# Kernel optimization log

Hardware: AMD Instinct MI355X
Metric: run time of the kernel (lower is better)

The kernel has to match this reference:

```python
import jax, jax.numpy as jnp
import numpy as np
from jax.scipy.linalg import cholesky, solve_triangular, cho_solve

N, M, D = 16384, 2048, 8
VAR, LS = 1.0, 0.5      # RBF kernel hyperparameters (same for kernel_f and kernel_g)
JITTER = 1e-6
BATCH_RATE = 1.0
HALF_LOG_2PI = 0.5 * float(np.log(2.0 * np.pi))


def rbf(x1, x2):
    # K[i,j] = VAR * exp(-||x1_i - x2_j||^2 / (2 LS^2))
    d2 = (jnp.sum(x1 * x1, 1)[:, None] + jnp.sum(x2 * x2, 1)[None, :]
          - 2.0 * (x1 @ x2.T))
    return VAR * jnp.exp(-0.5 * d2 / (LS * LS))


def setup_inputs() -> dict:
    key = jax.random.key(0)
    ks = jax.random.split(key, 7)
    x = jax.random.normal(ks[0], (N, D), dtype=jnp.float32)
    y = jax.random.normal(ks[1], (N, 1), dtype=jnp.float32)
    z = 2.0 * jax.random.uniform(ks[2], (M, D), dtype=jnp.float32) - 1.0  # inducing inputs in [-1,1]^D
    q_m_f = 0.5 * jax.random.normal(ks[3], (M, 1), dtype=jnp.float32)
    q_m_g = 0.5 * jax.random.normal(ks[4], (M, 1), dtype=jnp.float32)
    # Cholesky-like params: identity plus small strictly-lower noise -> PD covariance
    q_L_f = jnp.eye(M, dtype=jnp.float32) + 0.01 * jnp.tril(
        jax.random.normal(ks[5], (M, M), dtype=jnp.float32), -1)
    q_L_g = jnp.eye(M, dtype=jnp.float32) + 0.01 * jnp.tril(
        jax.random.normal(ks[6], (M, M), dtype=jnp.float32), -1)
    return {"x": x, "y": y, "z": z, "q_m_f": q_m_f, "q_L_f": q_L_f,
            "q_m_g": q_m_g, "q_L_g": q_L_g}


def _gp_marginals_and_kl(x, z, q_m, q_L_raw):
    """Marginal posterior mean/var at x and KL(q(u)||p(u)) for one sparse GP."""
    L_S = jnp.tril(q_L_raw)                     # [M,M]
    Kuu = rbf(z, z) + JITTER * jnp.eye(M, dtype=x.dtype)
    Lk = cholesky(Kuu, lower=True)
    Kfu = rbf(x, z)                             # [N,M]
    # A = Kfu @ Kuu^{-1}
    A = cho_solve((Lk, True), Kfu.T).T          # [N,M]
    m = (A @ q_m)[:, 0]                         # [N]
    # diag(Kff + A (S - Kuu) A^T) = diag(Kff) + diag(A S A^T) - diag(Kfu A^T)
    S = L_S @ L_S.T
    diag_Kff = jnp.full((x.shape[0],), VAR, dtype=x.dtype)
    v = diag_Kff + jnp.sum((A @ S) * A, axis=1) - jnp.sum(A * Kfu, axis=1)
    # KL(N(q_m, S) || N(0, Kuu))
    alpha = solve_triangular(Lk, q_m, lower=True)       # Kuu^{-1/2} m
    W = solve_triangular(Lk, L_S, lower=True)           # Kuu^{-1/2} L_S
    logdet_K = 2.0 * jnp.sum(jnp.log(jnp.diag(Lk)))
    logdet_S = 2.0 * jnp.sum(jnp.log(jnp.abs(jnp.diag(L_S))))
    kl = 0.5 * (jnp.sum(W * W) + jnp.sum(alpha * alpha)
                - jnp.asarray(M, x.dtype) + logdet_K - logdet_S)
    return m, v, kl


def reference(x, y, z, q_m_f, q_L_f, q_m_g, q_L_g):
    m_f, v_f, kl_f = _gp_marginals_and_kl(x, z, q_m_f, q_L_f)
    m_g, v_g, kl_g = _gp_marginals_and_kl(x, z, q_m_g, q_L_g)
    yv = y[:, 0]
    # HetGaussian variational expectation (Saul et al. 2016):
    # E_q[log N(y | f, exp(g))] per point
    expectation = (-HALF_LOG_2PI - 0.5 * m_g
                   - 0.5 * ((yv - m_f) ** 2 + v_f) * jnp.exp(-m_g + 0.5 * v_g))
    elbo = BATCH_RATE * jnp.sum(expectation) - (kl_f + kl_g)
    return -elbo
```

## Files before the change

kernel.cpp:

```cpp
#include <hip/hip_runtime.h>
#include <math.h>

#define NN 16384
#define MM 2048
#define DD 8
#define NB 32
#define GRIDN 256
#define SZB ((size_t)16777216)

constexpr float HLOG2PI = 0.91893853320467274178f;

using short8  = __attribute__((ext_vector_type(8))) short;
using float4v = __attribute__((ext_vector_type(4))) float;

__device__ __forceinline__ float4v f4zero(){ float4v v; v[0]=0.f; v[1]=0.f; v[2]=0.f; v[3]=0.f; return v; }

__device__ __forceinline__ void bfsplit(float v, short& h, short& lo){
  unsigned b = __float_as_uint(v);
  h = (short)(b >> 16);
  float hf = __uint_as_float(b & 0xFFFF0000u);
  lo = (short)(__float_as_uint(v - hf) >> 16);
}
__device__ __forceinline__ float bf2f(short s){
  return __uint_as_float(((unsigned)(unsigned short)s) << 16);
}
__device__ __forceinline__ float4v mfma3(short8 ah, short8 al, short8 bh, short8 bl, float4v c){
  c = __builtin_amdgcn_mfma_f32_16x16x32_bf16(ah, bh, c, 0, 0, 0);
  c = __builtin_amdgcn_mfma_f32_16x16x32_bf16(ah, bl, c, 0, 0, 0);
  c = __builtin_amdgcn_mfma_f32_16x16x32_bf16(al, bh, c, 0, 0, 0);
  return c;
}

__device__ __forceinline__ void gbar(int* cnt, int* flag, int& gen){
  __syncthreads();
  if (threadIdx.x == 0){
    ++gen;
    __builtin_amdgcn_fence(__ATOMIC_RELEASE, "agent");
    int old = __hip_atomic_fetch_add(cnt, 1, __ATOMIC_RELAXED, __HIP_MEMORY_SCOPE_AGENT);
    if (old == gen*GRIDN - 1){
      __builtin_amdgcn_fence(__ATOMIC_ACQ_REL, "agent");
      __hip_atomic_store(flag, gen, __ATOMIC_RELAXED, __HIP_MEMORY_SCOPE_AGENT);
    } else {
      while (__hip_atomic_load(flag, __ATOMIC_RELAXED, __HIP_MEMORY_SCOPE_AGENT) < gen)
        __builtin_amdgcn_s_sleep(8);
    }
    __builtin_amdgcn_fence(__ATOMIC_ACQUIRE, "agent");
  }
  __syncthreads();
}

__device__ __forceinline__ float block_reduce(float v, float* scratch){
  int lane = threadIdx.x & 63;
  int w    = threadIdx.x >> 6;
  #pragma unroll
  for (int off=32; off; off>>=1) v += __shfl_down(v, off, 64);
  __syncthreads();
  if (lane==0) scratch[w] = v;
  __syncthreads();
  float r = 0.f;
  if (threadIdx.x < 4) r = scratch[threadIdx.x];
  if (w==0){ r += __shfl_down(r, 2, 64); r += __shfl_down(r, 1, 64); }
  return r;
}

__device__ __forceinline__ void stage64(float (*S)[68], const float* __restrict__ g, int ld, int t){
  #pragma unroll
  for (int p=t; p<1024; p+=256)
    *(float4*)&S[p>>4][(p&15)*4] = *(const float4*)&g[(size_t)(p>>4)*ld + (p&15)*4];
}
__device__ __forceinline__ void tile_gemm_step(float acc[4][4], const float (*As)[68], const float (*Bs)[68], int tx, int ty){
  for (int k=0;k<64;++k){
    float ar[4], bc4[4];
    #pragma unroll
    for (int u=0;u<4;++u){ ar[u]=As[ty*4+u][k]; bc4[u]=Bs[k][tx*4+u]; }
    #pragma unroll
    for (int u=0;u<4;++u)
      #pragma unroll
      for (int v=0;v<4;++v) acc[u][v] += ar[u]*bc4[v];
  }
}
__device__ __forceinline__ void tile_syrk_step(float acc[4][4], const float (*P)[68], const float (*Q)[68], int tx, int ty){
  for (int k=0;k<64;++k){
    float pr[4], qc[4];
    #pragma unroll
    for (int u=0;u<4;++u){ pr[u]=P[ty*4+u][k]; qc[u]=Q[tx*4+u][k]; }
    #pragma unroll
    for (int u=0;u<4;++u)
      #pragma unroll
      for (int v=0;v<4;++v) acc[u][v] += pr[u]*qc[v];
  }
}

__device__ void factor64(float (*A)[68], float* __restrict__ lkd, float* __restrict__ sdg_, int d, int t){
  for (int j=0;j<64;++j){
    float ajj = A[j][j];
    float piv = sqrtf(fmaxf(ajj, 1e-20f));
    float rp  = 1.f/piv;
    float val = 0.f;
    if (t>j && t<64){ val = A[t][j]*rp; A[t][j]=val; }
    __syncthreads();
    if (t<64){
      if (t>j) for (int c=j+1;c<=t;++c) A[t][c] -= val*A[c][j];
      if (t==j){ A[j][j]=piv; sdg_[d*64+j]=rp; }
    }
    __syncthreads();
  }
  for (int p=t; p<4096; p+=256){ int i=p>>6, c=p&63;
    lkd[d*4096+p] = (c<=i)? A[i][c] : 0.f; }
}

__global__ __launch_bounds__(256) void factor_coop(
    const float* __restrict__ z,
    const float* __restrict__ qlf, const float* __restrict__ qlg,
    const float* __restrict__ qmf, const float* __restrict__ qmg,
    float* __restrict__ kuu, float* __restrict__ linv,
    float* __restrict__ wf, float* __restrict__ wg,
    float* __restrict__ af, float* __restrict__ ag,
    float* __restrict__ ptmp, float* __restrict__ lkdiag,
    float* __restrict__ sdg, int* __restrict__ cnt, int* __restrict__ flag)
{
  __shared__ float As[64][68];
  __shared__ float Bs[64][68];
  __shared__ float sd[64];
  const int bid = blockIdx.x, t = threadIdx.x;
  const int tx = t & 15, ty = t >> 4;
  int gen = 0;

  if (bid == 0){
    for (int p=t; p<128; p+=256){ int i=p>>1, h=p&1;
      *(float4*)&As[i][h*4] = *(const float4*)&z[(size_t)i*DD + h*4]; }
    __syncthreads();
    float kv[4][4];
    #pragma unroll
    for (int u=0;u<4;++u)
      #pragma unroll
      for (int v=0;v<4;++v){
        float d2=0.f;
        #pragma unroll
        for (int d=0;d<8;++d){ float df=As[ty*4+u][d]-As[tx*4+v][d]; d2+=df*df; }
        kv[u][v] = __expf(-2.f*d2) + ((ty*4+u)==(tx*4+v) ? 1e-6f : 0.f);
      }
    __syncthreads();
    #pragma unroll
    for (int u=0;u<4;++u)
      #pragma unroll
      for (int v=0;v<4;++v) As[ty*4+u][tx*4+v] = kv[u][v];
    __syncthreads();
    factor64(As, lkdiag, sdg, 0, t);
  } else {
    for (int idx=bid; idx<528; idx+=GRIDN-1){
      int r=0; while ((r+1)*(r+2)/2 <= idx) ++r;
      int c = idx - r*(r+1)/2;
      __syncthreads();
      for (int p=t; p<128; p+=256){ int i=p>>1, h=p&1;
        *(float4*)&As[i][h*4] = *(const float4*)&z[(size_t)(r*64+i)*DD + h*4];
        *(float4*)&Bs[i][h*4] = *(const float4*)&z[(size_t)(c*64+i)*DD + h*4]; }
      __syncthreads();
      #pragma unroll
      for (int u=0;u<4;++u){
        float4 o;
        float* ov = (float*)&o;
        #pragma unroll
        for (int v=0;v<4;++v){
          float d2=0.f;
          #pragma unroll
          for (int d=0;d<8;++d){ float df=As[ty*4+u][d]-Bs[tx*4+v][d]; d2+=df*df; }
          float val = __expf(-2.f*d2);
          if (r*64+ty*4+u == c*64+tx*4+v) val += 1e-6f;
          ov[v] = val;
        }
        *(float4*)&kuu[(size_t)(r*64+ty*4+u)*MM + c*64 + tx*4] = o;
      }
    }
  }
  gbar(cnt, flag, gen);

  for (int kb=0; kb<31; ++kb){
    int R = MM - (kb+1)*64;
    int nact = (R + 255) >> 8;
    if (bid < nact){
      for (int p=t; p<1024; p+=256)
        *(float4*)&As[p>>4][(p&15)*4] = *(const float4*)&lkdiag[kb*4096 + p*4];
      if (t < 64) sd[t] = sdg[kb*64 + t];
      __syncthreads();
      int row = (kb+1)*64 + bid*256 + t;
      if (row < MM){
        float xr[64];
        float* ap = kuu + (size_t)row*MM + kb*64;
        #pragma unroll
        for (int c4=0; c4<16; ++c4) *(float4*)&xr[c4*4] = *(const float4*)&ap[c4*4];
        #pragma unroll
        for (int j=0; j<64; ++j){
          float xj = xr[j]*sd[j];
          xr[j] = xj;
          #pragma unroll
          for (int c=j+1; c<64; ++c) xr[c] -= xj*As[c][j];
        }
        #pragma unroll
        for (int c4=0; c4<16; ++c4) *(float4*)&ap[c4*4] = *(float4*)&xr[c4*4];
      }
    }
    gbar(cnt, flag, gen);

    int T = NB-1 - kb;
    int ntiles = T*(T+1)/2;
    if (bid == 0){
      int bi = kb+1;
      stage64(As, kuu + (size_t)(bi*64)*MM + kb*64, MM, t);
      __syncthreads();
      float acc[4][4] = {};
      tile_syrk_step(acc, As, As, tx, ty);
      __syncthreads();
      #pragma unroll
      for (int u=0;u<4;++u)
        #pragma unroll
        for (int v=0;v<4;++v) Bs[ty*4+u][tx*4+v] = acc[u][v];
      __syncthreads();
      for (int p=t;p<1024;p+=256){
        int i=p>>4, c4=p&15;
        float4 kv = *(const float4*)&kuu[(size_t)(bi*64+i)*MM + bi*64 + c4*4];
        float4 bv = *(float4*)&Bs[i][c4*4];
        float4 o; o.x=kv.x-bv.x; o.y=kv.y-bv.y; o.z=kv.z-bv.z; o.w=kv.w-bv.w;
        *(float4*)&As[i][c4*4] = o;
      }
      __syncthreads();
      factor64(As, lkdiag, sdg, kb+1, t);
    } else {
      for (int idx=bid; idx<ntiles; idx+=GRIDN-1){
        int r=0; while ((r+1)*(r+2)/2 <= idx) ++r;
        int c = idx - r*(r+1)/2;
        int bi = kb+1+r, bc = kb+1+c;
        __syncthreads();
        stage64(As, kuu + (size_t)(bi*64)*MM + kb*64, MM, t);
        stage64(Bs, kuu + (size_t)(bc*64)*MM + kb*64, MM, t);
        __syncthreads();
        float acc[4][4] = {};
        tile_syrk_step(acc, As, Bs, tx, ty);
        #pragma unroll
        for (int u=0;u<4;++u){
          float4* dst = (float4*)&kuu[(size_t)(bi*64+ty*4+u)*MM + bc*64 + tx*4];
          float4 o = *dst;
          o.x-=acc[u][0]; o.y-=acc[u][1]; o.z-=acc[u][2]; o.w-=acc[u][3];
          *dst = o;
        }
      }
    }
    gbar(cnt, flag, gen);
  }

  if (bid < NB){
    stage64(As, lkdiag + bid*4096, 64, t);
    __syncthreads();
    if (t < 64){
      for (int j=0;j<64;++j){
        float s = (j==t)?1.f:0.f;
        for (int k=t;k<j;++k) s -= As[j][k]*Bs[k][t];
        Bs[j][t] = (j>=t)? s/As[j][j] : 0.f;
      }
    }
    __syncthreads();
    for (int p=t;p<1024;p+=256){ int i=p>>4, c4=p&15;
      *(float4*)&linv[(size_t)(bid*64+i)*MM + bid*64 + c4*4] = *(float4*)&Bs[i][c4*4]; }
  }
  gbar(cnt, flag, gen);

  for (int s=0; s<5; ++s){
    int nb = 1<<s, mc = 16>>s, b = 64<<s;
    int tiles = mc*nb*nb;
    for (int idx=bid; idx<tiles; idx+=GRIDN){
      int m = idx/(nb*nb), r2 = idx%(nb*nb);
      int ti = r2/nb, tj = r2%nb;
      int rb = m*2*nb + nb + ti, cb0 = m*2*nb;
      float acc[4][4]={};
      for (int k=tj; k<nb; ++k){
        __syncthreads();
        stage64(As, kuu  + (size_t)(rb*64)*MM + (cb0+k)*64, MM, t);
        stage64(Bs, linv + (size_t)((cb0+k)*64)*MM + (cb0+tj)*64, MM, t);
        __syncthreads();
        tile_gemm_step(acc, As, Bs, tx, ty);
      }
      float* pm = ptmp + (size_t)m*b*b;
      #pragma unroll
      for (int u=0;u<4;++u)
        *(float4*)&pm[(size_t)(ti*64+ty*4+u)*b + tj*64 + tx*4] =
            make_float4(acc[u][0],acc[u][1],acc[u][2],acc[u][3]);
    }
    gbar(cnt, flag, gen);
    for (int idx=bid; idx<tiles; idx+=GRIDN){
      int m = idx/(nb*nb), r2 = idx%(nb*nb);
      int ti = r2/nb, tj = r2%nb;
      int rb = m*2*nb + nb + ti;
      const float* pm = ptmp + (size_t)m*b*b;
      float acc[4][4]={};
      for (int k=0; k<=ti; ++k){
        __syncthreads();
        stage64(As, linv + (size_t)(rb*64)*MM + (m*2*nb+nb+k)*64, MM, t);
        stage64(Bs, pm + (size_t)(k*64)*b + tj*64, b, t);
        __syncthreads();
        tile_gemm_step(acc, As, Bs, tx, ty);
      }
      #pragma unroll
      for (int u=0;u<4;++u)
        *(float4*)&linv[(size_t)(rb*64+ty*4+u)*MM + (m*2*nb+tj)*64 + tx*4] =
            make_float4(-acc[u][0],-acc[u][1],-acc[u][2],-acc[u][3]);
    }
    gbar(cnt, flag, gen);
  }

  for (int idx=bid; idx<2*528; idx+=GRIDN){
    int gp = idx/528, rem = idx%528;
    int bi=0; while ((bi+1)*(bi+2)/2 <= rem) ++bi;
    int bj = rem - bi*(bi+1)/2;
    const float* ql = gp ? qlg : qlf;
    float* w        = gp ? wg  : wf;
    float acc[4][4]={};
    for (int bk=bj; bk<=bi; ++bk){
      __syncthreads();
      stage64(As, linv + (size_t)(bi*64)*MM + bk*64, MM, t);
      stage64(Bs, ql   + (size_t)(bk*64)*MM + bj*64, MM, t);
      __syncthreads();
      if (bk==bj){
        for (int p=t;p<4096;p+=256){ int i=p>>6, c=p&63; if (i<c) Bs[i][c]=0.f; }
        __syncthreads();
      }
      tile_gemm_step(acc, As, Bs, tx, ty);
    }
    #pragma unroll
    for (int u=0;u<4;++u)
      *(float4*)&w[(size_t)(bi*64+ty*4+u)*MM + bj*64 + tx*4] =
          make_float4(acc[u][0],acc[u][1],acc[u][2],acc[u][3]);
  }
  {
    int gw = bid*4 + (t>>6), l = t&63;
    for (int job=gw; job<4096; job+=GRIDN*4){
      int gp = job>>11, r = job&2047;
      const float* qm = gp ? qmg : qmf;
      float s=0.f;
      for (int c=l; c<=r; c+=64) s += linv[(size_t)r*MM+c]*qm[c];
      #pragma unroll
      for (int off=32; off; off>>=1) s += __shfl_down(s, off, 64);
      if (l==0) (gp ? ag : af)[r] = s;
    }
  }
}


__global__ __launch_bounds__(256) void zfrag_kernel(const float* __restrict__ z,
    short* __restrict__ zfh, short* __restrict__ zfl, float* __restrict__ zn2){
  int zr = blockIdx.x*256 + threadIdx.x;
  float v[DD]; float s = 0.f;
  #pragma unroll
  for (int d=0; d<DD; ++d){ v[d] = z[zr*DD + d]; s += v[d]*v[d]; }
  zn2[zr] = s;
  size_t base = (size_t)(zr >> 4)*512 + (zr & 15)*32;
  #pragma unroll
  for (int k=0; k<32; ++k){
    short h = 0, lo = 0;
    if (k < DD) bfsplit(v[k], h, lo);
    zfh[base + k] = h; zfl[base + k] = lo;
  }
}

__global__ __launch_bounds__(256) void red_small(const float* __restrict__ lkd,
    const float* __restrict__ qlf, const float* __restrict__ qlg,
    const float* __restrict__ af, const float* __restrict__ ag,
    float* __restrict__ scal){
  __shared__ float scratch[4];
  float ldk=0, ldf=0, ldg=0, a2f=0, a2g=0;
  for (int i=threadIdx.x;i<MM;i+=256){
    int kb = i>>6, r = i&63;
    ldk += __logf(lkd[kb*4096 + r*64 + r]);
    ldf += __logf(fabsf(qlf[(size_t)i*MM+i]));
    ldg += __logf(fabsf(qlg[(size_t)i*MM+i]));
    float v = af[i]; a2f += v*v;
    v = ag[i];       a2g += v*v;
  }
  float r;
  r = block_reduce(ldk, scratch); if (threadIdx.x==0) scal[0] = 2.f*r;
  r = block_reduce(ldf, scratch); if (threadIdx.x==0) scal[1] = 2.f*r;
  r = block_reduce(ldg, scratch); if (threadIdx.x==0) scal[2] = 2.f*r;
  r = block_reduce(a2f, scratch); if (threadIdx.x==0) scal[3] = r;
  r = block_reduce(a2g, scratch); if (threadIdx.x==0) scal[4] = r;
}

__global__ __launch_bounds__(256) void redw_kernel(const float* __restrict__ wf,
    const float* __restrict__ wg, float* __restrict__ scal){
  __shared__ float scratch[4];
  size_t start  = (size_t)blockIdx.x*256 + threadIdx.x;
  size_t stride = (size_t)gridDim.x*256;
  float sf=0, sg=0;
  for (size_t p=start;p<(size_t)MM*MM;p+=stride){
    float v=wf[p]; sf += v*v;
    v=wg[p];       sg += v*v;
  }
  float r = block_reduce(sf, scratch);
  if (threadIdx.x==0) atomicAdd(&scal[5], r);
  r = block_reduce(sg, scratch);
  if (threadIdx.x==0) atomicAdd(&scal[6], r);
}

__global__ void kl_kernel(const float* __restrict__ scal, float* __restrict__ out){
  float klf = 0.5f*(scal[5] + scal[3] - (float)MM + scal[0] - scal[1]);
  float klg = 0.5f*(scal[6] + scal[4] - (float)MM + scal[0] - scal[2]);
  out[0] += klf + klg;
}

__global__ __launch_bounds__(256) void split_rowmajor(const float* __restrict__ src,
    short* __restrict__ dh, short* __restrict__ dl){
  int p = blockIdx.x*256 + threadIdx.x;
  int chunk = p >> 9, wi = p & 511;
  int mo = chunk >> 6, ko = chunk & 63;
  int row = mo*16 + (wi >> 5), col = ko*32 + (wi & 31);
  float v = src[(size_t)row*MM + col];
  short h, lo; bfsplit(v, h, lo);
  dh[p] = h; dl[p] = lo;
}

__global__ __launch_bounds__(256) void split_transpose(const float* __restrict__ src,
    short* __restrict__ dh, short* __restrict__ dl){
  __shared__ float tile[32][33];
  int t = threadIdx.x;
  int mb = blockIdx.x, kb = blockIdx.y;
  #pragma unroll
  for (int k=0;k<4;++k){
    int idx = t + k*256;
    int lr = idx >> 5, lc = idx & 31;
    tile[lr][lc] = src[(size_t)(kb*32+lr)*MM + mb*32 + lc];
  }
  __syncthreads();
  #pragma unroll
  for (int e=0;e<4;++e){
    int p = t*4 + e;
    int c = p >> 9, wi = p & 511;
    int i = (wi >> 5) & 15, kk = wi & 31;
    float v = tile[kk][c*16 + i];
    short h, lo; bfsplit(v, h, lo);
    size_t gp = ((size_t)(mb*2 + c)*64 + kb)*512 + wi;
    dh[gp] = h; dl[gp] = lo;
  }
}

__global__ __launch_bounds__(256, 2) void tt_mfma(
    const float* __restrict__ x, const float* __restrict__ zn2,
    const short* __restrict__ zfh, const short* __restrict__ zfl,
    const short* __restrict__ lvh, const short* __restrict__ lvl,
    short* __restrict__ tth, short* __restrict__ ttl){
  __shared__ __align__(16) short lAh[8192], lAl[8192], lBh[8192], lBl[8192];
  int t = threadIdx.x;
  int l = t & 63, w = t >> 6;
  int istrip = blockIdx.x, bj2 = blockIdx.y;
  int li = l & 15, q = l >> 4;
  int lofs = li*32 + q*8;
  int wn4 = (w>>1)*4, wm4 = (w&1)*4;

  short8 xh[2], xl[2];
  float xn2v[8];
  {
    float xn2t[2];
    #pragma unroll
    for (int tn=0; tn<2; ++tn){
      int n = istrip*128 + w*32 + tn*16 + li;
      const float4* xp = (const float4*)(x + (size_t)n*DD);
      float4 p0 = xp[0], p1 = xp[1];
      float v[8] = {p0.x,p0.y,p0.z,p0.w,p1.x,p1.y,p1.z,p1.w};
      float s = 0.f;
      #pragma unroll
      for (int d=0; d<8; ++d) s += v[d]*v[d];
      xn2t[tn] = s;
      short8 hh, ll;
      #pragma unroll
      for (int j=0; j<8; ++j){
        short h=0, lo=0;
        if (q==0) bfsplit(v[j], h, lo);
        hh[j]=h; ll[j]=lo;
      }
      xh[tn]=hh; xl[tn]=ll;
    }
    #pragma unroll
    for (int tn=0; tn<2; ++tn)
      #pragma unroll
      for (int r=0; r<4; ++r)
        xn2v[tn*4+r] = __shfl(xn2t[tn], q*4 + r, 64);
  }

  float4v acc[4][4];
  #pragma unroll
  for (int i=0;i<4;++i)
    #pragma unroll
    for (int j=0;j<4;++j) acc[i][j] = f4zero();

  int nkt = 2*bj2 + 2;
  for (int bk=0; bk<nkt; ++bk){
    __syncthreads();
    {
      short8 zh[4], zl[4];
      float zt2[4];
      #pragma unroll
      for (int tz=0; tz<4; ++tz){
        size_t zo = (size_t)(bk*4 + tz)*512 + lofs;
        zh[tz] = *(const short8*)(zfh + zo);
        zl[tz] = *(const short8*)(zfl + zo);
        zt2[tz] = zn2[bk*64 + tz*16 + li];
      }
      #pragma unroll
      for (int tn=0; tn<2; ++tn){
        #pragma unroll
        for (int tz=0; tz<4; ++tz){
          float4v s4 = mfma3(xh[tn], xl[tn], zh[tz], zl[tz], f4zero());
          #pragma unroll
          for (int r=0; r<4; ++r){
            float e = __expf(4.f*s4[r] - 2.f*(xn2v[tn*4+r] + zt2[tz]));
            short h, lo; bfsplit(e, h, lo);
            int pos = ((w*2+tn)*2 + (tz>>1))*512 + (q*4+r)*32 + (tz&1)*16 + li;
            lAh[pos] = h; lAl[pos] = lo;
          }
        }
      }
    }
    #pragma unroll
    for (int c4 = t; c4 < 1024; c4 += 256){
      int ch = c4 >> 6, wdi = c4 & 63;
      size_t g = ((size_t)(bj2*8 + (ch>>1))*64 + (size_t)(bk*2 + (ch&1)))*64 + wdi;
      ((uint4*)lBh)[c4] = ((const uint4*)lvh)[g];
      ((uint4*)lBl)[c4] = ((const uint4*)lvl)[g];
    }
    __syncthreads();
    #pragma unroll
    for (int s=0; s<2; ++s){
      short8 ah[4], al[4], bh[4], bl[4];
      #pragma unroll
      for (int tn=0; tn<4; ++tn){
        int off = ((wn4+tn)*2 + s)*512 + lofs;
        ah[tn] = *(const short8*)&lAh[off];
        al[tn] = *(const short8*)&lAl[off];
      }
      #pragma unroll
      for (int tm=0; tm<4; ++tm){
        int off = ((wm4+tm)*2 + s)*512 + lofs;
        bh[tm] = *(const short8*)&lBh[off];
        bl[tm] = *(const short8*)&lBl[off];
      }
      #pragma unroll
      for (int tn=0; tn<4; ++tn)
        #pragma unroll
        for (int tm=0; tm<4; ++tm)
          acc[tn][tm] = mfma3(ah[tn], al[tn], bh[tm], bl[tm], acc[tn][tm]);
    }
  }
  #pragma unroll
  for (int tn=0; tn<4; ++tn){
    int no_g = istrip*8 + wn4 + tn;
    #pragma unroll
    for (int tm=0; tm<4; ++tm){
      int mo_g = bj2*4 + (w&1)*2 + (tm>>1);
      size_t cb = ((size_t)no_g*64 + mo_g)*512;
      #pragma unroll
      for (int r=0; r<4; ++r){
        short h, lo; bfsplit(acc[tn][tm][r], h, lo);
        size_t pos = cb + (q*4+r)*32 + (tm&1)*16 + li;
        tth[pos] = h; ttl[pos] = lo;
      }
    }
  }
}

__global__ __launch_bounds__(256) void lin_v2(const short* __restrict__ tth,
    const short* __restrict__ ttl, const float* __restrict__ af, const float* __restrict__ ag,
    float* __restrict__ t2, float* __restrict__ lf, float* __restrict__ lg){
  int t = threadIdx.x;
  int w = t >> 6, l = t & 63;
  int n = blockIdx.x*4 + w;
  int g = l >> 2, j = l & 3;
  float s2=0.f, sf=0.f, sg=0.f;
  #pragma unroll
  for (int it=0; it<4; ++it){
    int ck = g + it*16;
    size_t off = ((size_t)(n>>4)*64 + ck)*512 + (n&15)*32 + j*8;
    short8 h8 = *(const short8*)(tth + off);
    short8 l8 = *(const short8*)(ttl + off);
    int m0 = ck*32 + j*8;
    float4 a0 = *(const float4*)(af + m0), a1 = *(const float4*)(af + m0 + 4);
    float4 g0 = *(const float4*)(ag + m0), g1 = *(const float4*)(ag + m0 + 4);
    float av[8] = {a0.x,a0.y,a0.z,a0.w,a1.x,a1.y,a1.z,a1.w};
    float gv[8] = {g0.x,g0.y,g0.z,g0.w,g1.x,g1.y,g1.z,g1.w};
    #pragma unroll
    for (int e=0; e<8; ++e){
      float tv = bf2f(h8[e]) + bf2f(l8[e]);
      s2 += tv*tv; sf += tv*av[e]; sg += tv*gv[e];
    }
  }
  #pragma unroll
  for (int off=32; off; off>>=1){
    s2 += __shfl_down(s2, off, 64);
    sf += __shfl_down(sf, off, 64);
    sg += __shfl_down(sg, off, 64);
  }
  if (l==0){ t2[n] = s2; lf[n] = sf; lg[n] = sg; }
}

__global__ __launch_bounds__(256, 2) void quad_mfma(
    const short* __restrict__ tth, const short* __restrict__ ttl,
    const short* __restrict__ wfh, const short* __restrict__ wfl,
    const short* __restrict__ wgh, const short* __restrict__ wgl,
    float* __restrict__ vfq, float* __restrict__ vgq){
  __shared__ __align__(16) short lAh[8192], lAl[8192], lBh[8192], lBl[8192];
  int t = threadIdx.x, l = t & 63, w = t >> 6;
  int istrip = blockIdx.x, bj2 = blockIdx.y;
  const short* gbh = blockIdx.z ? wgh : wfh;
  const short* gbl = blockIdx.z ? wgl : wfl;
  float* vq = blockIdx.z ? vgq : vfq;
  int li = l & 15, q = l >> 4;
  int lofs = li*32 + q*8;
  int wn4 = (w>>1)*4, wm4 = (w&1)*4;

  float4v acc[4][4];
  #pragma unroll
  for (int i=0;i<4;++i)
    #pragma unroll
    for (int j=0;j<4;++j) acc[i][j] = f4zero();

  for (int bk=2*bj2; bk<32; ++bk){
    __syncthreads();
    #pragma unroll
    for (int c4 = t; c4 < 1024; c4 += 256){
      int ch = c4 >> 6, wdi = c4 & 63;
      size_t ga = ((size_t)(istrip*8 + (ch>>1))*64 + (size_t)(bk*2 + (ch&1)))*64 + wdi;
      ((uint4*)lAh)[c4] = ((const uint4*)tth)[ga];
      ((uint4*)lAl)[c4] = ((const uint4*)ttl)[ga];
      size_t gb = ((size_t)(bj2*8 + (ch>>1))*64 + (size_t)(bk*2 + (ch&1)))*64 + wdi;
      ((uint4*)lBh)[c4] = ((const uint4*)gbh)[gb];
      ((uint4*)lBl)[c4] = ((const uint4*)gbl)[gb];
    }
    __syncthreads();
    #pragma unroll
    for (int s=0; s<2; ++s){
      short8 ah[4], al[4], bh[4], bl[4];
      #pragma unroll
      for (int tn=0; tn<4; ++tn){
        int off = ((wn4+tn)*2 + s)*512 + lofs;
        ah[tn] = *(const short8*)&lAh[off];
        al[tn] = *(const short8*)&lAl[off];
      }
      #pragma unroll
      for (int tm=0; tm<4; ++tm){
        int off = ((wm4+tm)*2 + s)*512 + lofs;
        bh[tm] = *(const short8*)&lBh[off];
        bl[tm] = *(const short8*)&lBl[off];
      }
      #pragma unroll
      for (int tn=0; tn<4; ++tn)
        #pragma unroll
        for (int tm=0; tm<4; ++tm)
          acc[tn][tm] = mfma3(ah[tn], al[tn], bh[tm], bl[tm], acc[tn][tm]);
    }
  }
  float rs[16];
  #pragma unroll
  for (int tn=0; tn<4; ++tn)
    #pragma unroll
    for (int r=0; r<4; ++r){
      float s = 0.f;
      #pragma unroll
      for (int tm=0; tm<4; ++tm){ float v = acc[tn][tm][r]; s += v*v; }
      rs[tn*4+r] = s;
    }
  #pragma unroll
  for (int off=8; off; off>>=1)
    #pragma unroll
    for (int k=0; k<16; ++k) rs[k] += __shfl_down(rs[k], off, 16);
  if (li == 0){
    #pragma unroll
    for (int tn=0; tn<4; ++tn)
      #pragma unroll
      for (int r=0; r<4; ++r){
        int n = istrip*128 + (w>>1)*64 + tn*16 + q*4 + r;
        atomicAdd(&vq[n], rs[tn*4+r]);
      }
  }
}

__global__ __launch_bounds__(256) void final_kernel(const float* __restrict__ y,
    const float* __restrict__ t2, const float* __restrict__ lf, const float* __restrict__ lg,
    const float* __restrict__ vfq, const float* __restrict__ vgq, float* __restrict__ out){
  __shared__ float scratch[4];
  int i = blockIdx.x*256 + threadIdx.x;
  float mf = lf[i], mg = lg[i];
  float vf = 1.f + vfq[i] - t2[i];
  float vg = 1.f + vgq[i] - t2[i];
  float dy = y[i] - mf;
  float e = -HLOG2PI - 0.5f*mg - 0.5f*(dy*dy + vf)*__expf(-mg + 0.5f*vg);
  float r = block_reduce(e, scratch);
  if (threadIdx.x==0) atomicAdd(out, -r);
}

extern "C" void kernel_launch(void* const* d_in, const int* in_sizes, int n_in,
                              void* d_out, int out_size, void* d_ws, size_t ws_size,
                              hipStream_t stream){
  (void)in_sizes; (void)n_in; (void)out_size; (void)ws_size;
  const float* x   = (const float*)d_in[0];
  const float* y   = (const float*)d_in[1];
  const float* z   = (const float*)d_in[2];
  const float* qmf = (const float*)d_in[3];
  const float* qlf = (const float*)d_in[4];
  const float* qmg = (const float*)d_in[5];
  const float* qlg = (const float*)d_in[6];
  float* out = (float*)d_out;
  char* Bw = (char*)d_ws;

  float* kuu  = (float*)Bw;
  float* linv = (float*)(Bw + SZB);
  float* wf   = (float*)(Bw + 2*SZB);
  float* wg   = (float*)(Bw + 3*SZB);
  short* lvh  = (short*)Bw;
  short* lvl  = (short*)(Bw + SZB/2);
  short* wfh  = (short*)(Bw + SZB);
  short* wfl  = (short*)(Bw + SZB + SZB/2);
  short* wgh  = (short*)(Bw + 2*SZB);
  short* wgl  = (short*)(Bw + 2*SZB + SZB/2);
  short* tth  = (short*)(Bw + 3*SZB);
  short* ttl  = (short*)(Bw + 3*SZB + (size_t)NN*MM*2);
  float* ptmp   = (float*)(Bw + 4*SZB);
  float* lkdiag = (float*)(Bw + 4*SZB + (size_t)4194304);
  float* sdg    = (float*)(Bw + 4*SZB + (size_t)4194304 + (size_t)524288);
  float* sm   = (float*)(Bw + 3*SZB + (size_t)NN*MM*4);
  float* af = sm;          float* ag = af + MM;
  float* t2 = ag + MM;     float* lf = t2 + NN;   float* lg = lf + NN;
  float* vfq = lg + NN;    float* vgq = vfq + NN; float* scal = vgq + NN;
  int*   cnt  = (int*)(scal + 8);
  int*   flag = (int*)(scal + 40);
  float* zn2 = scal + 48;
  short* zfh = (short*)(zn2 + MM);
  short* zfl = zfh + MM*32;

  hipMemsetAsync(out, 0, sizeof(float), stream);
  hipMemsetAsync(vfq, 0, (size_t)(2*NN + 48)*sizeof(float), stream);
  hipMemsetAsync(wf,  0, 2*SZB, stream);
  hipMemsetAsync(linv,0, SZB,   stream);

  zfrag_kernel<<<MM/256, 256, 0, stream>>>(z, zfh, zfl, zn2);

  factor_coop<<<GRIDN, 256, 0, stream>>>(z, qlf, qlg, qmf, qmg,
                                         kuu, linv, wf, wg, af, ag,
                                         ptmp, lkdiag, sdg, cnt, flag);

  red_small<<<1, 256, 0, stream>>>(lkdiag, qlf, qlg, af, ag, scal);
  redw_kernel<<<512, 256, 0, stream>>>(wf, wg, scal);
  kl_kernel<<<1, 1, 0, stream>>>(scal, out);

  split_rowmajor<<<MM*MM/256, 256, 0, stream>>>(linv, lvh, lvl);
  split_transpose<<<dim3(MM/32, MM/32), 256, 0, stream>>>(wf, wfh, wfl);
  split_transpose<<<dim3(MM/32, MM/32), 256, 0, stream>>>(wg, wgh, wgl);

  tt_mfma<<<dim3(NN/128, MM/128), 256, 0, stream>>>(x, zn2, zfh, zfl, lvh, lvl, tth, ttl);
  lin_v2<<<NN/4, 256, 0, stream>>>(tth, ttl, af, ag, t2, lf, lg);
  quad_mfma<<<dim3(NN/128, MM/128, 2), 256, 0, stream>>>(tth, ttl, wfh, wfl, wgh, wgl, vfq, vgq);
  final_kernel<<<NN/256, 256, 0, stream>>>(y, t2, lf, lg, vfq, vgq, out);
}
```

Measured before the change: 4.743 ms.

## Use hierarchical per-XCD grid barrier, register Cholesky diag, dedicated first inverse level

Replaces the flat global atomic grid barrier with a two-level barrier that first counts blocks per XCD (read from the hardware XCC_ID register) and then across XCDs. This cuts contention on a single counter across the many barriers of the cooperative Cholesky kernel. It also rewrites the 64x64 diagonal block factorization to run in registers with wave shuffles instead of shared memory with per-column syncthreads, and computes the first level of the triangular-inverse recursion with a specialized two-GEMM tile path, which removes one barrier. The cost is a startup barrier used to discover block placement, plus reliance on the hardware register read.

```diff
diff --git a/kernel.cpp b/kernel.cpp
--- a/kernel.cpp
+++ b/kernel.cpp
@@ -31,7 +31,8 @@
   return c;
 }
 
-__device__ __forceinline__ void gbar(int* cnt, int* flag, int& gen){
+
+__device__ __forceinline__ void gbar0(int* cnt, int* flag, int& gen){
   __syncthreads();
   if (threadIdx.x == 0){
     ++gen;
@@ -49,6 +50,35 @@
   __syncthreads();
 }
 
+__device__ __forceinline__ void gbar_h(int* bar, int xcc, int myN, int nxcd, int& gen){
+  __syncthreads();
+  if (threadIdx.x == 0){
+    ++gen;
+    int* lcnt  = bar + xcc*32;
+    int* lflag = bar + 512 + xcc*32;
+    int* gcnt  = bar + 1024;
+    int* gflag = bar + 1056;
+    int old = __hip_atomic_fetch_add(lcnt, 1, __ATOMIC_RELAXED, __HIP_MEMORY_SCOPE_AGENT);
+    if (old == gen*myN - 1){
+      __builtin_amdgcn_fence(__ATOMIC_RELEASE, "agent");
+      int g = __hip_atomic_fetch_add(gcnt, 1, __ATOMIC_RELAXED, __HIP_MEMORY_SCOPE_AGENT);
+      if (g == gen*nxcd - 1){
+        __hip_atomic_store(gflag, gen, __ATOMIC_RELAXED, __HIP_MEMORY_SCOPE_AGENT);
+      } else {
+        while (__hip_atomic_load(gflag, __ATOMIC_RELAXED, __HIP_MEMORY_SCOPE_AGENT) < gen)
+          __builtin_amdgcn_s_sleep(2);
+      }
+      __builtin_amdgcn_fence(__ATOMIC_ACQUIRE, "agent");
+      __hip_atomic_store(lflag, gen, __ATOMIC_RELAXED, __HIP_MEMORY_SCOPE_AGENT);
+    } else {
+      while (__hip_atomic_load(lflag, __ATOMIC_RELAXED, __HIP_MEMORY_SCOPE_AGENT) < gen)
+        __builtin_amdgcn_s_sleep(4);
+      __builtin_amdgcn_fence(__ATOMIC_ACQUIRE, "agent");
+    }
+  }
+  __syncthreads();
+}
+
 __device__ __forceinline__ float block_reduce(float v, float* scratch){
   int lane = threadIdx.x & 63;
   int w    = threadIdx.x >> 6;
@@ -91,22 +121,35 @@
   }
 }
 
-__device__ void factor64(float (*A)[68], float* __restrict__ lkd, float* __restrict__ sdg_, int d, int t){
-  for (int j=0;j<64;++j){
-    float ajj = A[j][j];
-    float piv = sqrtf(fmaxf(ajj, 1e-20f));
-    float rp  = 1.f/piv;
-    float val = 0.f;
-    if (t>j && t<64){ val = A[t][j]*rp; A[t][j]=val; }
-    __syncthreads();
-    if (t<64){
-      if (t>j) for (int c=j+1;c<=t;++c) A[t][c] -= val*A[c][j];
-      if (t==j){ A[j][j]=piv; sdg_[d*64+j]=rp; }
-    }
-    __syncthreads();
-  }
-  for (int p=t; p<4096; p+=256){ int i=p>>6, c=p&63;
-    lkd[d*4096+p] = (c<=i)? A[i][c] : 0.f; }
+__device__ __forceinline__ void factor64_reg(const float (*S)[68],
+    float* __restrict__ lkd, float* __restrict__ sdg_, int d, int t){
+  if (t < 64){
+    float xr[64];
+    #pragma unroll
+    for (int c4=0;c4<16;++c4) *(float4*)&xr[c4*4] = *(const float4*)&S[t][c4*4];
+    float myrp = 1.f;
+    #pragma unroll
+    for (int j=0;j<64;++j){
+      float ajj = __shfl(xr[j], j, 64);
+      float piv = sqrtf(fmaxf(ajj, 1e-20f));
+      float rp  = 1.f/piv;
+      float val = xr[j]*rp;
+      if (t==j){ xr[j] = piv; myrp = rp; }
+      else if (t>j) xr[j] = val;
+      else val = 0.f;
+      #pragma unroll
+      for (int c=j+1;c<64;++c){
+        float vc = __shfl(val, c, 64);
+        if (c<=t) xr[c] -= val*vc;
+      }
+    }
+    #pragma unroll
+    for (int c=0;c<64;++c) if (c>t) xr[c] = 0.f;
+    #pragma unroll
+    for (int c4=0;c4<16;++c4)
+      *(float4*)&lkd[d*4096 + t*64 + c4*4] = *(float4*)&xr[c4*4];
+    sdg_[d*64 + t] = myrp;
+  }
 }
 
 __global__ __launch_bounds__(256) void factor_coop(
@@ -117,13 +160,31 @@
     float* __restrict__ wf, float* __restrict__ wg,
     float* __restrict__ af, float* __restrict__ ag,
     float* __restrict__ ptmp, float* __restrict__ lkdiag,
-    float* __restrict__ sdg, int* __restrict__ cnt, int* __restrict__ flag)
+    float* __restrict__ sdg, int* __restrict__ bar)
 {
   __shared__ float As[64][68];
   __shared__ float Bs[64][68];
   __shared__ float sd[64];
+  __shared__ int binfo[2];
   const int bid = blockIdx.x, t = threadIdx.x;
   const int tx = t & 15, ty = t >> 4;
+
+  int xcc_r;
+  asm volatile("s_getreg_b32 %0, hwreg(HW_REG_XCC_ID)" : "=s"(xcc_r));
+  const int xcc = xcc_r & 15;
+  if (t == 0)
+    __hip_atomic_fetch_add(bar + 1152 + xcc*32, 1, __ATOMIC_RELAXED, __HIP_MEMORY_SCOPE_AGENT);
+  int gen0 = 0;
+  gbar0(bar + 1088, bar + 1120, gen0);
+  if (t == 0){
+    int myN = __hip_atomic_load(bar + 1152 + xcc*32, __ATOMIC_RELAXED, __HIP_MEMORY_SCOPE_AGENT);
+    int nx = 0;
+    for (int i=0;i<16;++i)
+      nx += (__hip_atomic_load(bar + 1152 + i*32, __ATOMIC_RELAXED, __HIP_MEMORY_SCOPE_AGENT) > 0);
+    binfo[0] = myN; binfo[1] = nx;
+  }
+  __syncthreads();
+  const int myN = binfo[0], nxcd = binfo[1];
   int gen = 0;
 
   if (bid == 0){
@@ -146,7 +207,7 @@
       #pragma unroll
       for (int v=0;v<4;++v) As[ty*4+u][tx*4+v] = kv[u][v];
     __syncthreads();
-    factor64(As, lkdiag, sdg, 0, t);
+    factor64_reg(As, lkdiag, sdg, 0, t);
   } else {
     for (int idx=bid; idx<528; idx+=GRIDN-1){
       int r=0; while ((r+1)*(r+2)/2 <= idx) ++r;
@@ -173,7 +234,7 @@
       }
     }
   }
-  gbar(cnt, flag, gen);
+  gbar_h(bar, xcc, myN, nxcd, gen);
 
   for (int kb=0; kb<31; ++kb){
     int R = MM - (kb+1)*64;
@@ -200,7 +261,7 @@
         for (int c4=0; c4<16; ++c4) *(float4*)&ap[c4*4] = *(float4*)&xr[c4*4];
       }
     }
-    gbar(cnt, flag, gen);
+    gbar_h(bar, xcc, myN, nxcd, gen);
 
     int T = NB-1 - kb;
     int ntiles = T*(T+1)/2;
@@ -224,7 +285,7 @@
         *(float4*)&As[i][c4*4] = o;
       }
       __syncthreads();
-      factor64(As, lkdiag, sdg, kb+1, t);
+      factor64_reg(As, lkdiag, sdg, kb+1, t);
     } else {
       for (int idx=bid; idx<ntiles; idx+=GRIDN-1){
         int r=0; while ((r+1)*(r+2)/2 <= idx) ++r;
@@ -245,7 +306,7 @@
         }
       }
     }
-    gbar(cnt, flag, gen);
+    gbar_h(bar, xcc, myN, nxcd, gen);
   }
 
   if (bid < NB){
@@ -262,9 +323,33 @@
     for (int p=t;p<1024;p+=256){ int i=p>>4, c4=p&15;
       *(float4*)&linv[(size_t)(bid*64+i)*MM + bid*64 + c4*4] = *(float4*)&Bs[i][c4*4]; }
   }
-  gbar(cnt, flag, gen);
-
-  for (int s=0; s<5; ++s){
+  gbar_h(bar, xcc, myN, nxcd, gen);
+
+  for (int idx=bid; idx<16; idx+=GRIDN){
+    int m = idx;
+    __syncthreads();
+    stage64(As, kuu  + (size_t)((2*m+1)*64)*MM + (2*m)*64, MM, t);
+    stage64(Bs, linv + (size_t)((2*m)*64)*MM   + (2*m)*64, MM, t);
+    __syncthreads();
+    float acc[4][4]={};
+    tile_gemm_step(acc, As, Bs, tx, ty);
+    __syncthreads();
+    #pragma unroll
+    for (int u=0;u<4;++u)
+      #pragma unroll
+      for (int v=0;v<4;++v) Bs[ty*4+u][tx*4+v] = acc[u][v];
+    stage64(As, linv + (size_t)((2*m+1)*64)*MM + (2*m+1)*64, MM, t);
+    __syncthreads();
+    float o[4][4]={};
+    tile_gemm_step(o, As, Bs, tx, ty);
+    #pragma unroll
+    for (int u=0;u<4;++u)
+      *(float4*)&linv[(size_t)((2*m+1)*64+ty*4+u)*MM + (2*m)*64 + tx*4] =
+          make_float4(-o[u][0],-o[u][1],-o[u][2],-o[u][3]);
+  }
+  gbar_h(bar, xcc, myN, nxcd, gen);
+
+  for (int s=1; s<5; ++s){
     int nb = 1<<s, mc = 16>>s, b = 64<<s;
     int tiles = mc*nb*nb;
     for (int idx=bid; idx<tiles; idx+=GRIDN){
@@ -285,7 +370,7 @@
         *(float4*)&pm[(size_t)(ti*64+ty*4+u)*b + tj*64 + tx*4] =
             make_float4(acc[u][0],acc[u][1],acc[u][2],acc[u][3]);
     }
-    gbar(cnt, flag, gen);
+    gbar_h(bar, xcc, myN, nxcd, gen);
     for (int idx=bid; idx<tiles; idx+=GRIDN){
       int m = idx/(nb*nb), r2 = idx%(nb*nb);
       int ti = r2/nb, tj = r2%nb;
@@ -304,7 +389,7 @@
         *(float4*)&linv[(size_t)(rb*64+ty*4+u)*MM + (m*2*nb+tj)*64 + tx*4] =
             make_float4(-acc[u][0],-acc[u][1],-acc[u][2],-acc[u][3]);
     }
-    gbar(cnt, flag, gen);
+    gbar_h(bar, xcc, myN, nxcd, gen);
   }
 
   for (int idx=bid; idx<2*528; idx+=GRIDN){
@@ -726,14 +811,13 @@
   float* af = sm;          float* ag = af + MM;
   float* t2 = ag + MM;     float* lf = t2 + NN;   float* lg = lf + NN;
   float* vfq = lg + NN;    float* vgq = vfq + NN; float* scal = vgq + NN;
-  int*   cnt  = (int*)(scal + 8);
-  int*   flag = (int*)(scal + 40);
-  float* zn2 = scal + 48;
+  int*   bar = (int*)(scal + 64);
+  float* zn2 = scal + 64 + 2048;
   short* zfh = (short*)(zn2 + MM);
   short* zfl = zfh + MM*32;
 
   hipMemsetAsync(out, 0, sizeof(float), stream);
-  hipMemsetAsync(vfq, 0, (size_t)(2*NN + 48)*sizeof(float), stream);
+  hipMemsetAsync(vfq, 0, (size_t)(2*NN + 64 + 2048)*sizeof(float), stream);
   hipMemsetAsync(wf,  0, 2*SZB, stream);
   hipMemsetAsync(linv,0, SZB,   stream);
 
@@ -741,7 +825,7 @@
 
   factor_coop<<<GRIDN, 256, 0, stream>>>(z, qlf, qlg, qmf, qmg,
                                          kuu, linv, wf, wg, af, ag,
-                                         ptmp, lkdiag, sdg, cnt, flag);
+                                         ptmp, lkdiag, sdg, bar);
 
   red_small<<<1, 256, 0, stream>>>(lkdiag, qlf, qlg, af, ag, scal);
   redw_kernel<<<512, 256, 0, stream>>>(wf, wg, scal);
```

Result: slower. 4.873 ms (+2.7%).
